# Optimization experiments

Hardware: AMD Instinct MI355X
Metric: run time of the kernel (lower is better)

## Reference

```python
import jax, jax.numpy as jnp
import numpy as np

B, V, L, C, H = 2, 8, 256, 1024, 16

def setup_inputs() -> dict:
    key = jax.random.key(0)
    ks = jax.random.split(key, 6)
    s = 0.02  # init scale for weights
    x = jax.random.normal(ks[0], (B, V, L, C), jnp.float32)
    Wq = jax.random.normal(ks[1], (C, C), jnp.float32) * s
    Wk = jax.random.normal(ks[2], (C, C), jnp.float32) * s
    Wv = jax.random.normal(ks[3], (C, C), jnp.float32) * s
    Wp = jax.random.normal(ks[4], (C, C), jnp.float32) * s
    bp = jnp.zeros((C,), jnp.float32)
    return {"x": x, "Wq": Wq, "Wk": Wk, "Wv": Wv, "Wp": Wp, "bp": bp}

def _view_mask(V, L):
    # view-level allow mask, expanded to token level [S, S]
    vi = jnp.arange(V)
    qv, kv = vi[:, None], vi[None, :]
    cross = ((qv == 0) & (kv == 1)) | ((qv == 1) & (kv == 0))
    later = (qv > 1) | (kv > 1)
    allow = cross | (later & (qv >= kv))  # [V, V]
    return jnp.repeat(jnp.repeat(allow, L, axis=0), L, axis=1)  # [V*L, V*L]

def reference(x, Wq, Wk, Wv, Wp, bp):
    b, v, l, c = x.shape
    h = H
    dh = c // h
    scale = dh ** -0.5
    s = v * l
    xf = x.reshape(b, s, c)
    # torch Linear: y = x @ W.T
    q = (xf @ Wq.T).reshape(b, s, h, dh).transpose(0, 2, 1, 3)  # [b,h,s,dh]
    k = (xf @ Wk.T).reshape(b, s, h, dh).transpose(0, 2, 1, 3)
    vv = (xf @ Wv.T).reshape(b, s, h, dh).transpose(0, 2, 1, 3)
    scores = jnp.einsum('bhqd,bhkd->bhqk', q, k) * scale  # [b,h,s,s]
    mask = _view_mask(v, l)
    scores = jnp.where(mask, scores, -jnp.inf)
    attn = jax.nn.softmax(scores, axis=-1)
    out = jnp.einsum('bhqk,bhkd->bhqd', attn, vv)
    out = out.transpose(0, 2, 1, 3).reshape(b, v, l, c)
    return out @ Wp.T + bp
```

## Files before the change

kernel.cpp:

```cpp
#include <hip/hip_runtime.h>
#include <stdint.h>

typedef unsigned short ushort_t;
typedef __attribute__((ext_vector_type(8))) __bf16 bf16x8;
typedef __attribute__((ext_vector_type(4))) float floatx4;
typedef __attribute__((ext_vector_type(2))) uint32_t uint32x2;

__device__ __forceinline__ ushort_t f2bf(float f) {
    uint32_t u = __builtin_bit_cast(uint32_t, f);
    u += 0x7fffu + ((u >> 16) & 1u);
    return (ushort_t)(u >> 16);
}

typedef __attribute__((address_space(1))) const void glb_void;
typedef __attribute__((address_space(3))) void lds_void;
__device__ __forceinline__ void gld16(const void* g, void* l) {
    __builtin_amdgcn_global_load_lds((glb_void*)g, (lds_void*)l, 16, 0, 0);
}

#define QSCALE 0.18033688011112042f

__global__ void cast_kernel(const float* __restrict__ x,
                            const float* __restrict__ Wq, const float* __restrict__ Wk,
                            const float* __restrict__ Wv, const float* __restrict__ Wp,
                            ushort_t* __restrict__ xb, ushort_t* __restrict__ Wqkvb,
                            ushort_t* __restrict__ Wpb)
{
    const int64_t NX = 4194304, NW = 1048576;
    int64_t i4 = ((int64_t)blockIdx.x * blockDim.x + threadIdx.x) * 4;
    const float* src; ushort_t* dst; int64_t off;
    if (i4 < NX)            { src = x;  dst = xb;          off = i4; }
    else if (i4 < NX+NW)    { src = Wq; dst = Wqkvb;       off = i4 - NX; }
    else if (i4 < NX+2*NW)  { src = Wk; dst = Wqkvb + NW;  off = i4 - NX - NW; }
    else if (i4 < NX+3*NW)  { src = Wv; dst = Wqkvb + 2*NW;off = i4 - NX - 2*NW; }
    else                    { src = Wp; dst = Wpb;         off = i4 - NX - 3*NW; }
    float4 v = *(const float4*)(src + off);
    ushort4 o;
    o.x = f2bf(v.x); o.y = f2bf(v.y); o.z = f2bf(v.z); o.w = f2bf(v.w);
    *(ushort4*)(dst + off) = o;
}

#define BM 128
#define BN 128
#define BK 32

__global__ __launch_bounds__(256, 3)
void gemm_bt(const ushort_t* __restrict__ A, const ushort_t* __restrict__ Bmat,
             int M, int N, int K, int mode,
             ushort_t* __restrict__ qb, ushort_t* __restrict__ kb, ushort_t* __restrict__ vtb,
             float* __restrict__ outf, const float* __restrict__ bias)
{
    __shared__ ushort_t As[BM * BK];
    __shared__ ushort_t Bs[BN * BK];
    const int tid  = threadIdx.x;
    const int lane = tid & 63;
    const int wave = tid >> 6;
    const int m0 = blockIdx.x * BM;
    const int n0 = blockIdx.y * BN;
    const int wrow = (wave >> 1) * 64;
    const int wcol = (wave & 1) * 64;
    const int q_ = lane >> 4;
    const int ml = lane & 15;

    floatx4 acc[4][4];
    for (int i = 0; i < 4; i++) for (int j = 0; j < 4; j++) acc[i][j] = floatx4{0.f,0.f,0.f,0.f};

    const int t0 = wave * 2, t1 = wave * 2 + 1;
    const int row_l = lane >> 2;
    const int col_l = (lane & 3) * 8;
    const ushort_t* Ag0 = A    + (int64_t)(m0 + t0*16 + row_l) * K + col_l;
    const ushort_t* Ag1 = A    + (int64_t)(m0 + t1*16 + row_l) * K + col_l;
    const ushort_t* Bg0 = Bmat + (int64_t)(n0 + t0*16 + row_l) * K + col_l;
    const ushort_t* Bg1 = Bmat + (int64_t)(n0 + t1*16 + row_l) * K + col_l;
    ushort_t* Al0 = As + t0*512; ushort_t* Al1 = As + t1*512;
    ushort_t* Bl0 = Bs + t0*512; ushort_t* Bl1 = Bs + t1*512;

    for (int k0 = 0; k0 < K; k0 += BK) {
        __syncthreads();
        gld16(Ag0 + k0, Al0);
        gld16(Ag1 + k0, Al1);
        gld16(Bg0 + k0, Bl0);
        gld16(Bg1 + k0, Bl1);
        __syncthreads();
        bf16x8 af[4], bf[4];
        for (int mt = 0; mt < 4; mt++)
            af[mt] = *(const bf16x8*)(As + (wrow + mt*16 + ml) * BK + q_*8);
        for (int nt = 0; nt < 4; nt++)
            bf[nt] = *(const bf16x8*)(Bs + (wcol + nt*16 + ml) * BK + q_*8);
        for (int mt = 0; mt < 4; mt++)
            for (int nt = 0; nt < 4; nt++)
                acc[mt][nt] = __builtin_amdgcn_mfma_f32_16x16x32_bf16(af[mt], bf[nt], acc[mt][nt], 0, 0, 0);
    }

    if (mode == 0) {
        for (int mt = 0; mt < 4; mt++) for (int nt = 0; nt < 4; nt++) {
            floatx4 v = acc[mt][nt];
            int col = n0 + wcol + nt*16 + ml;
            int which = col >> 10;
            int nn = col & 1023;
            int h = nn >> 6, d = nn & 63;
            if (which < 2) {
                ushort_t* dst = (which == 0) ? qb : kb;
                float sc = (which == 0) ? QSCALE : 1.0f;
                for (int r = 0; r < 4; r++) {
                    int rowg = m0 + wrow + mt*16 + q_*4 + r;
                    int b = rowg >> 11, s = rowg & 2047;
                    dst[(((int64_t)(b*16 + h) * 2048 + s) << 6) + d] = f2bf(v[r] * sc);
                }
            } else {
                int rowg0 = m0 + wrow + mt*16 + q_*4;
                int b = rowg0 >> 11, sbase = rowg0 & 2047;
                ushort4 o;
                o.x = f2bf(v[0]); o.y = f2bf(v[1]); o.z = f2bf(v[2]); o.w = f2bf(v[3]);
                *(ushort4*)(vtb + (((int64_t)(b*16 + h) * 64 + d) << 11) + sbase) = o;
            }
        }
    } else {
        for (int mt = 0; mt < 4; mt++) for (int nt = 0; nt < 4; nt++) {
            floatx4 v = acc[mt][nt];
            int col = n0 + wcol + nt*16 + ml;
            float bv = bias[col];
            for (int r = 0; r < 4; r++) {
                int rowg = m0 + wrow + mt*16 + q_*4 + r;
                outf[(int64_t)rowg * N + col] = v[r] + bv;
            }
        }
    }
}

__global__ __launch_bounds__(256, 2)
void attn_kernel(const ushort_t* __restrict__ Q, const ushort_t* __restrict__ Kb,
                 const ushort_t* __restrict__ Vt, ushort_t* __restrict__ Out)
{
    __shared__ ushort_t Kl[8192];
    __shared__ ushort_t Vl[8192];
    __shared__ ushort_t Pl[4 * 32 * 136];

    int bi = blockIdx.x;
    int bh = (bi & 7) + 8 * ((bi >> 3) & 3);
    int qt = (bi >> 5) & 1;
    int g8 = bi >> 6;
    int qv = (g8 < 4) ? (7 - g8) : (g8 - 4);
    int b = bh >> 4, h = bh & 15;
    int tid = threadIdx.x;
    int wave = tid >> 6, lane = tid & 63;
    int q_ = lane >> 4, ml = lane & 15;
    int rlane = lane & 15, clane = lane >> 4;
    int s0 = qv*256 + qt*128 + wave*32;

    const ushort_t* Kbh = Kb + ((int64_t)bh << 17);
    const ushort_t* Vbh = Vt + ((int64_t)bh << 17);
    ushort_t* Pw = Pl + wave * (32 * 136);

    const ushort_t* Qp = Q + (((int64_t)bh*2048 + s0 + ml) << 6) + q_*8;
    bf16x8 aq0A = *(const bf16x8*)(Qp);
    bf16x8 aq1A = *(const bf16x8*)(Qp + 32);
    bf16x8 aq0B = *(const bf16x8*)(Qp + 1024);
    bf16x8 aq1B = *(const bf16x8*)(Qp + 1024 + 32);

    floatx4 o_accA[4], o_accB[4];
    for (int i = 0; i < 4; i++) { o_accA[i] = floatx4{0.f,0.f,0.f,0.f};
                                  o_accB[i] = floatx4{0.f,0.f,0.f,0.f}; }
    float lsumA = 0.f, lsumB = 0.f;

    int views[8]; int nviews;
    if      (qv == 0) { views[0] = 1; nviews = 1; }
    else if (qv == 1) { views[0] = 0; nviews = 1; }
    else { nviews = qv + 1; for (int i = 0; i < nviews; i++) views[i] = i; }

    for (int vi = 0; vi < nviews; vi++) {
        int kb0 = views[vi] * 256;
        for (int ck = 0; ck < 2; ck++) {
            int koff = kb0 + ck * 128;

            __syncthreads();
            #pragma unroll
            for (int i = 0; i < 4; i++) {
                int id = wave*4 + i;
                const ushort_t* gk = Kbh + (((int64_t)(koff + (id >> 1)*16 + rlane)) << 6)
                                         + (id & 1)*32 + clane*8;
                gld16(gk, Kl + id*512);
                const ushort_t* gv = Vbh + ((int64_t)((id & 3)*16 + rlane) << 11)
                                         + koff + (id >> 2)*32 + clane*8;
                gld16(gv, Vl + id*512);
            }
            __syncthreads();

            #pragma unroll
            for (int kt = 0; kt < 8; kt++) {
                bf16x8 k0 = *(const bf16x8*)(Kl + kt*1024 + lane*8);
                bf16x8 k1 = *(const bf16x8*)(Kl + kt*1024 + 512 + lane*8);
                floatx4 czA = floatx4{0.f,0.f,0.f,0.f};
                floatx4 czB = floatx4{0.f,0.f,0.f,0.f};
                __builtin_amdgcn_s_setprio(1);
                czA = __builtin_amdgcn_mfma_f32_16x16x32_bf16(k0, aq0A, czA, 0, 0, 0);
                czA = __builtin_amdgcn_mfma_f32_16x16x32_bf16(k1, aq1A, czA, 0, 0, 0);
                czB = __builtin_amdgcn_mfma_f32_16x16x32_bf16(k0, aq0B, czB, 0, 0, 0);
                czB = __builtin_amdgcn_mfma_f32_16x16x32_bf16(k1, aq1B, czB, 0, 0, 0);
                __builtin_amdgcn_s_setprio(0);

                float a0 = __builtin_amdgcn_exp2f(czA[0]);
                float a1 = __builtin_amdgcn_exp2f(czA[1]);
                float a2 = __builtin_amdgcn_exp2f(czA[2]);
                float a3 = __builtin_amdgcn_exp2f(czA[3]);
                lsumA += (a0 + a1) + (a2 + a3);
                uint32x2 wa;
                wa[0] = (uint32_t)f2bf(a0) | ((uint32_t)f2bf(a1) << 16);
                wa[1] = (uint32_t)f2bf(a2) | ((uint32_t)f2bf(a3) << 16);
                *(uint32x2*)(Pw + ml*136 + kt*16 + q_*4) = wa;

                float b0 = __builtin_amdgcn_exp2f(czB[0]);
                float b1 = __builtin_amdgcn_exp2f(czB[1]);
                float b2 = __builtin_amdgcn_exp2f(czB[2]);
                float b3 = __builtin_amdgcn_exp2f(czB[3]);
                lsumB += (b0 + b1) + (b2 + b3);
                uint32x2 wb;
                wb[0] = (uint32_t)f2bf(b0) | ((uint32_t)f2bf(b1) << 16);
                wb[1] = (uint32_t)f2bf(b2) | ((uint32_t)f2bf(b3) << 16);
                *(uint32x2*)(Pw + (16 + ml)*136 + kt*16 + q_*4) = wb;
            }

            asm volatile("s_waitcnt lgkmcnt(0)" ::: "memory");

            #pragma unroll
            for (int g = 0; g < 4; g++) {
                bf16x8 apA = *(const bf16x8*)(Pw + ml*136 + g*32 + q_*8);
                bf16x8 apB = *(const bf16x8*)(Pw + (16 + ml)*136 + g*32 + q_*8);
                __builtin_amdgcn_s_setprio(1);
                #pragma unroll
                for (int dt = 0; dt < 4; dt++) {
                    bf16x8 vv = *(const bf16x8*)(Vl + (g*4 + dt)*512 + lane*8);
                    o_accA[dt] = __builtin_amdgcn_mfma_f32_16x16x32_bf16(apA, vv, o_accA[dt], 0, 0, 0);
                    o_accB[dt] = __builtin_amdgcn_mfma_f32_16x16x32_bf16(apB, vv, o_accB[dt], 0, 0, 0);
                }
                __builtin_amdgcn_s_setprio(0);
            }
        }
    }

    lsumA += __shfl_xor(lsumA, 16);
    lsumA += __shfl_xor(lsumA, 32);
    lsumB += __shfl_xor(lsumB, 16);
    lsumB += __shfl_xor(lsumB, 32);
    float rinvA[4], rinvB[4];
    #pragma unroll
    for (int r = 0; r < 4; r++) {
        rinvA[r] = 1.0f / __shfl(lsumA, q_*4 + r);
        rinvB[r] = 1.0f / __shfl(lsumB, q_*4 + r);
    }

    #pragma unroll
    for (int dt = 0; dt < 4; dt++)
        #pragma unroll
        for (int r = 0; r < 4; r++) {
            int srA = s0 + q_*4 + r;
            Out[((int64_t)b*2048 + srA) * 1024 + h*64 + dt*16 + ml] = f2bf(o_accA[dt][r] * rinvA[r]);
            int srB = s0 + 16 + q_*4 + r;
            Out[((int64_t)b*2048 + srB) * 1024 + h*64 + dt*16 + ml] = f2bf(o_accB[dt][r] * rinvB[r]);
        }
}

extern "C" void kernel_launch(void* const* d_in, const int* in_sizes, int n_in,
                              void* d_out, int out_size, void* d_ws, size_t ws_size,
                              hipStream_t stream) {
    const float* x  = (const float*)d_in[0];
    const float* Wq = (const float*)d_in[1];
    const float* Wk = (const float*)d_in[2];
    const float* Wv = (const float*)d_in[3];
    const float* Wp = (const float*)d_in[4];
    const float* bp = (const float*)d_in[5];
    float* out = (float*)d_out;

    char* ws = (char*)d_ws;
    ushort_t* xb    = (ushort_t*)(ws);
    ushort_t* Wqkvb = (ushort_t*)(ws + ((size_t)8  << 20));
    ushort_t* Wpb   = (ushort_t*)(ws + ((size_t)14 << 20));
    ushort_t* qb    = (ushort_t*)(ws + ((size_t)16 << 20));
    ushort_t* kbuf  = (ushort_t*)(ws + ((size_t)24 << 20));
    ushort_t* vtb   = (ushort_t*)(ws + ((size_t)40 << 20));
    ushort_t* attno = xb;

    cast_kernel<<<8192, 256, 0, stream>>>(x, Wq, Wk, Wv, Wp, xb, Wqkvb, Wpb);

    dim3 g0(4096 / BM, 3072 / BN);
    gemm_bt<<<g0, 256, 0, stream>>>(xb, Wqkvb, 4096, 3072, 1024, 0,
                                    qb, kbuf, vtb, nullptr, nullptr);

    attn_kernel<<<512, 256, 0, stream>>>(qb, kbuf, vtb, attno);

    dim3 g1(4096 / BM, 1024 / BN);
    gemm_bt<<<g1, 256, 0, stream>>>(attno, Wpb, 4096, 1024, 1024, 1,
                                    nullptr, nullptr, nullptr, out, bp);
}
```

Measured before the change: 189.8 us.

## Double-buffer K tiles and halve attention block size to 64 queries

The attention kernel now uses 128-thread blocks, each handling 64 query rows, launched as 1024 blocks instead of 512. K tiles are double-buffered in LDS so the next K chunk is prefetched while the current one is consumed. The V load for the next chunk is issued after the PV MFMAs, and explicit vmcnt waits plus raw s_barrier replace the full __syncthreads pairs. The aim is to hide global-to-LDS load latency and to improve load balance across the uneven per-view causal work. In exchange, each wave issues more loads and the hand-tuned vmcnt counts carry a risk of ordering bugs.

```diff
diff --git a/kernel.cpp b/kernel.cpp
--- a/kernel.cpp
+++ b/kernel.cpp
@@ -128,25 +128,25 @@
     }
 }
 
-__global__ __launch_bounds__(256, 2)
+__global__ __launch_bounds__(128, 2)
 void attn_kernel(const ushort_t* __restrict__ Q, const ushort_t* __restrict__ Kb,
                  const ushort_t* __restrict__ Vt, ushort_t* __restrict__ Out)
 {
-    __shared__ ushort_t Kl[8192];
+    __shared__ ushort_t Kd[2][8192];
     __shared__ ushort_t Vl[8192];
-    __shared__ ushort_t Pl[4 * 32 * 136];
+    __shared__ ushort_t Pl[2 * 32 * 136];
 
     int bi = blockIdx.x;
-    int bh = (bi & 7) + 8 * ((bi >> 3) & 3);
-    int qt = (bi >> 5) & 1;
-    int g8 = bi >> 6;
-    int qv = (g8 < 4) ? (7 - g8) : (g8 - 4);
+    int bh  = (bi & 7) + 8 * ((bi >> 3) & 3);
+    int qt2 = (bi >> 5) & 3;
+    int g8  = bi >> 7;
+    int qv  = (g8 < 6) ? (7 - g8) : (g8 - 6);
     int b = bh >> 4, h = bh & 15;
     int tid = threadIdx.x;
     int wave = tid >> 6, lane = tid & 63;
     int q_ = lane >> 4, ml = lane & 15;
     int rlane = lane & 15, clane = lane >> 4;
-    int s0 = qv*256 + qt*128 + wave*32;
+    int s0 = qv*256 + qt2*64 + wave*32;
 
     const ushort_t* Kbh = Kb + ((int64_t)bh << 17);
     const ushort_t* Vbh = Vt + ((int64_t)bh << 17);
@@ -163,77 +163,110 @@
                                   o_accB[i] = floatx4{0.f,0.f,0.f,0.f}; }
     float lsumA = 0.f, lsumB = 0.f;
 
-    int views[8]; int nviews;
-    if      (qv == 0) { views[0] = 1; nviews = 1; }
-    else if (qv == 1) { views[0] = 0; nviews = 1; }
-    else { nviews = qv + 1; for (int i = 0; i < nviews; i++) views[i] = i; }
-
-    for (int vi = 0; vi < nviews; vi++) {
-        int kb0 = views[vi] * 256;
-        for (int ck = 0; ck < 2; ck++) {
-            int koff = kb0 + ck * 128;
-
-            __syncthreads();
+    const int nviews = (qv < 2) ? 1 : (qv + 1);
+    const int NT = nviews * 2;
+    const int vfix = qv ^ 1;
+
+
+    {
+        int vw = (nviews == 1) ? vfix : 0;
+        int koff = vw * 256;
+        #pragma unroll
+        for (int i = 0; i < 8; i++) {
+            int id = wave*8 + i;
+            const ushort_t* gk = Kbh + (((int64_t)(koff + (id >> 1)*16 + rlane)) << 6)
+                                     + (id & 1)*32 + clane*8;
+            gld16(gk, Kd[0] + id*512);
+        }
+        #pragma unroll
+        for (int i = 0; i < 8; i++) {
+            int id = wave*8 + i;
+            const ushort_t* gv = Vbh + ((int64_t)((id & 3)*16 + rlane) << 11)
+                                     + koff + (id >> 2)*32 + clane*8;
+            gld16(gv, Vl + id*512);
+        }
+    }
+
+    for (int t = 0; t < NT; ++t) {
+        int cur = t & 1;
+        int koff = ((nviews == 1) ? vfix : (t >> 1)) * 256 + (t & 1) * 128;
+
+        if (t + 1 < NT) {
+            int koff_n = ((nviews == 1) ? vfix : ((t + 1) >> 1)) * 256 + ((t + 1) & 1) * 128;
             #pragma unroll
-            for (int i = 0; i < 4; i++) {
-                int id = wave*4 + i;
-                const ushort_t* gk = Kbh + (((int64_t)(koff + (id >> 1)*16 + rlane)) << 6)
+            for (int i = 0; i < 8; i++) {
+                int id = wave*8 + i;
+                const ushort_t* gk = Kbh + (((int64_t)(koff_n + (id >> 1)*16 + rlane)) << 6)
                                          + (id & 1)*32 + clane*8;
-                gld16(gk, Kl + id*512);
+                gld16(gk, Kd[cur ^ 1] + id*512);
+            }
+            asm volatile("s_waitcnt vmcnt(8)" ::: "memory");
+        } else {
+            asm volatile("s_waitcnt vmcnt(0)" ::: "memory");
+        }
+        __builtin_amdgcn_s_barrier();
+
+        const ushort_t* Kl = Kd[cur];
+        #pragma unroll
+        for (int kt = 0; kt < 8; kt++) {
+            bf16x8 k0 = *(const bf16x8*)(Kl + kt*1024 + lane*8);
+            bf16x8 k1 = *(const bf16x8*)(Kl + kt*1024 + 512 + lane*8);
+            floatx4 czA = floatx4{0.f,0.f,0.f,0.f};
+            floatx4 czB = floatx4{0.f,0.f,0.f,0.f};
+            __builtin_amdgcn_s_setprio(1);
+            czA = __builtin_amdgcn_mfma_f32_16x16x32_bf16(k0, aq0A, czA, 0, 0, 0);
+            czA = __builtin_amdgcn_mfma_f32_16x16x32_bf16(k1, aq1A, czA, 0, 0, 0);
+            czB = __builtin_amdgcn_mfma_f32_16x16x32_bf16(k0, aq0B, czB, 0, 0, 0);
+            czB = __builtin_amdgcn_mfma_f32_16x16x32_bf16(k1, aq1B, czB, 0, 0, 0);
+            __builtin_amdgcn_s_setprio(0);
+
+            float a0 = __builtin_amdgcn_exp2f(czA[0]);
+            float a1 = __builtin_amdgcn_exp2f(czA[1]);
+            float a2 = __builtin_amdgcn_exp2f(czA[2]);
+            float a3 = __builtin_amdgcn_exp2f(czA[3]);
+            lsumA += (a0 + a1) + (a2 + a3);
+            uint32x2 wa;
+            wa[0] = (uint32_t)f2bf(a0) | ((uint32_t)f2bf(a1) << 16);
+            wa[1] = (uint32_t)f2bf(a2) | ((uint32_t)f2bf(a3) << 16);
+            *(uint32x2*)(Pw + ml*136 + kt*16 + q_*4) = wa;
+
+            float b0 = __builtin_amdgcn_exp2f(czB[0]);
+            float b1 = __builtin_amdgcn_exp2f(czB[1]);
+            float b2 = __builtin_amdgcn_exp2f(czB[2]);
+            float b3 = __builtin_amdgcn_exp2f(czB[3]);
+            lsumB += (b0 + b1) + (b2 + b3);
+            uint32x2 wb;
+            wb[0] = (uint32_t)f2bf(b0) | ((uint32_t)f2bf(b1) << 16);
+            wb[1] = (uint32_t)f2bf(b2) | ((uint32_t)f2bf(b3) << 16);
+            *(uint32x2*)(Pw + (16 + ml)*136 + kt*16 + q_*4) = wb;
+        }
+
+        asm volatile("s_waitcnt lgkmcnt(0)" ::: "memory");
+
+        #pragma unroll
+        for (int g = 0; g < 4; g++) {
+            bf16x8 apA = *(const bf16x8*)(Pw + ml*136 + g*32 + q_*8);
+            bf16x8 apB = *(const bf16x8*)(Pw + (16 + ml)*136 + g*32 + q_*8);
+            __builtin_amdgcn_s_setprio(1);
+            #pragma unroll
+            for (int dt = 0; dt < 4; dt++) {
+                bf16x8 vv = *(const bf16x8*)(Vl + (g*4 + dt)*512 + lane*8);
+                o_accA[dt] = __builtin_amdgcn_mfma_f32_16x16x32_bf16(apA, vv, o_accA[dt], 0, 0, 0);
+                o_accB[dt] = __builtin_amdgcn_mfma_f32_16x16x32_bf16(apB, vv, o_accB[dt], 0, 0, 0);
+            }
+            __builtin_amdgcn_s_setprio(0);
+        }
+
+        __builtin_amdgcn_s_barrier();
+
+        if (t + 1 < NT) {
+            int koff_n = ((nviews == 1) ? vfix : ((t + 1) >> 1)) * 256 + ((t + 1) & 1) * 128;
+            #pragma unroll
+            for (int i = 0; i < 8; i++) {
+                int id = wave*8 + i;
                 const ushort_t* gv = Vbh + ((int64_t)((id & 3)*16 + rlane) << 11)
-                                         + koff + (id >> 2)*32 + clane*8;
+                                         + koff_n + (id >> 2)*32 + clane*8;
                 gld16(gv, Vl + id*512);
-            }
-            __syncthreads();
-
-            #pragma unroll
-            for (int kt = 0; kt < 8; kt++) {
-                bf16x8 k0 = *(const bf16x8*)(Kl + kt*1024 + lane*8);
-                bf16x8 k1 = *(const bf16x8*)(Kl + kt*1024 + 512 + lane*8);
-                floatx4 czA = floatx4{0.f,0.f,0.f,0.f};
-                floatx4 czB = floatx4{0.f,0.f,0.f,0.f};
-                __builtin_amdgcn_s_setprio(1);
-                czA = __builtin_amdgcn_mfma_f32_16x16x32_bf16(k0, aq0A, czA, 0, 0, 0);
-                czA = __builtin_amdgcn_mfma_f32_16x16x32_bf16(k1, aq1A, czA, 0, 0, 0);
-                czB = __builtin_amdgcn_mfma_f32_16x16x32_bf16(k0, aq0B, czB, 0, 0, 0);
-                czB = __builtin_amdgcn_mfma_f32_16x16x32_bf16(k1, aq1B, czB, 0, 0, 0);
-                __builtin_amdgcn_s_setprio(0);
-
-                float a0 = __builtin_amdgcn_exp2f(czA[0]);
-                float a1 = __builtin_amdgcn_exp2f(czA[1]);
-                float a2 = __builtin_amdgcn_exp2f(czA[2]);
-                float a3 = __builtin_amdgcn_exp2f(czA[3]);
-                lsumA += (a0 + a1) + (a2 + a3);
-                uint32x2 wa;
-                wa[0] = (uint32_t)f2bf(a0) | ((uint32_t)f2bf(a1) << 16);
-                wa[1] = (uint32_t)f2bf(a2) | ((uint32_t)f2bf(a3) << 16);
-                *(uint32x2*)(Pw + ml*136 + kt*16 + q_*4) = wa;
-
-                float b0 = __builtin_amdgcn_exp2f(czB[0]);
-                float b1 = __builtin_amdgcn_exp2f(czB[1]);
-                float b2 = __builtin_amdgcn_exp2f(czB[2]);
-                float b3 = __builtin_amdgcn_exp2f(czB[3]);
-                lsumB += (b0 + b1) + (b2 + b3);
-                uint32x2 wb;
-                wb[0] = (uint32_t)f2bf(b0) | ((uint32_t)f2bf(b1) << 16);
-                wb[1] = (uint32_t)f2bf(b2) | ((uint32_t)f2bf(b3) << 16);
-                *(uint32x2*)(Pw + (16 + ml)*136 + kt*16 + q_*4) = wb;
-            }
-
-            asm volatile("s_waitcnt lgkmcnt(0)" ::: "memory");
-
-            #pragma unroll
-            for (int g = 0; g < 4; g++) {
-                bf16x8 apA = *(const bf16x8*)(Pw + ml*136 + g*32 + q_*8);
-                bf16x8 apB = *(const bf16x8*)(Pw + (16 + ml)*136 + g*32 + q_*8);
-                __builtin_amdgcn_s_setprio(1);
-                #pragma unroll
-                for (int dt = 0; dt < 4; dt++) {
-                    bf16x8 vv = *(const bf16x8*)(Vl + (g*4 + dt)*512 + lane*8);
-                    o_accA[dt] = __builtin_amdgcn_mfma_f32_16x16x32_bf16(apA, vv, o_accA[dt], 0, 0, 0);
-                    o_accB[dt] = __builtin_amdgcn_mfma_f32_16x16x32_bf16(apB, vv, o_accB[dt], 0, 0, 0);
-                }
-                __builtin_amdgcn_s_setprio(0);
             }
         }
     }
@@ -286,7 +319,7 @@
     gemm_bt<<<g0, 256, 0, stream>>>(xb, Wqkvb, 4096, 3072, 1024, 0,
                                     qb, kbuf, vtb, nullptr, nullptr);
 
-    attn_kernel<<<512, 256, 0, stream>>>(qb, kbuf, vtb, attno);
+    attn_kernel<<<1024, 128, 0, stream>>>(qb, kbuf, vtb, attno);
 
     dim3 g1(4096 / BM, 1024 / BN);
     gemm_bt<<<g1, 256, 0, stream>>>(attno, Wpb, 4096, 1024, 1024, 1,
```

Measured after the change: 200.3 us. 1.06x slower.
